# Optimization experiments

Measured on AMD Instinct MI355X. Metric: run time of the kernel, lower is better.

## Reference

```python
import jax, jax.numpy as jnp
import numpy as np

# Repo globals / config
VOCAB_SIZE = 14
TOK_DIM = 8
POS_DIM = 8
D_MODEL = TOK_DIM + POS_DIM  # 16
MAX_SEQ_LEN = 2048
N_HEADS = 2
HEAD_DIM = 3
ATTN_DIM = N_HEADS * HEAD_DIM  # 6
FFN_DIM = 3
B, T = 16, 2048
EPS = 1e-5


def _ln(x, w, b):
    m = jnp.mean(x, axis=-1, keepdims=True)
    v = jnp.var(x, axis=-1, keepdims=True)
    return (x - m) * jax.lax.rsqrt(v + EPS) * w + b


def setup_inputs() -> dict:
    key = jax.random.key(0)
    ks = jax.random.split(key, 20)
    g = lambda k, shape: (jax.random.normal(k, shape, jnp.float32) * 0.1)
    return {
        "idx": jax.random.randint(ks[0], (B, T), 0, VOCAB_SIZE),
        "tok_emb": g(ks[1], (VOCAB_SIZE, TOK_DIM)),
        "pos_enc": g(ks[2], (MAX_SEQ_LEN, POS_DIM)),
        "Wq": g(ks[3], (ATTN_DIM, POS_DIM)),
        "Wk": g(ks[4], (ATTN_DIM, POS_DIM)),
        "Wv": g(ks[5], (ATTN_DIM, TOK_DIM)),
        "Wo": g(ks[6], (D_MODEL, ATTN_DIM)),
        "ln1_w": jnp.ones((D_MODEL,), jnp.float32),
        "ln1_b": jnp.zeros((D_MODEL,), jnp.float32),
        "ln2_w": jnp.ones((D_MODEL,), jnp.float32),
        "ln2_b": jnp.zeros((D_MODEL,), jnp.float32),
        "lnf_w": jnp.ones((D_MODEL,), jnp.float32),
        "lnf_b": jnp.zeros((D_MODEL,), jnp.float32),
        "W1": g(ks[7], (FFN_DIM, D_MODEL)),
        "b1": jnp.zeros((FFN_DIM,), jnp.float32),
        "W2": g(ks[8], (D_MODEL, FFN_DIM)),
        "b2": jnp.zeros((D_MODEL,), jnp.float32),
        "Wh": g(ks[9], (TOK_DIM, D_MODEL)),
    }


def reference(idx, tok_emb, pos_enc, Wq, Wk, Wv, Wo,
              ln1_w, ln1_b, ln2_w, ln2_b, lnf_w, lnf_b,
              W1, b1, W2, b2, Wh):
    Bq, Tq = idx.shape
    tok = tok_emb[idx]                                  # [B,T,TOK_DIM]
    pos = jnp.broadcast_to(pos_enc[:Tq][None], (Bq, Tq, POS_DIM))
    x = jnp.concatenate([tok, pos], axis=-1)            # [B,T,D_MODEL]
    h = _ln(x, ln1_w, ln1_b)
    x_tok = h[..., :TOK_DIM]
    x_pos = h[..., TOK_DIM:]
    # projections (torch Linear: y = x @ W.T)
    q = (x_pos @ Wq.T).reshape(Bq, Tq, N_HEADS, HEAD_DIM).transpose(0, 2, 1, 3)
    k = (x_pos @ Wk.T).reshape(Bq, Tq, N_HEADS, HEAD_DIM).transpose(0, 2, 1, 3)
    v = (x_tok @ Wv.T).reshape(Bq, Tq, N_HEADS, HEAD_DIM).transpose(0, 2, 1, 3)
    scores = jnp.einsum('bhqd,bhkd->bhqk', q, k) / jnp.sqrt(jnp.float32(HEAD_DIM))
    mask = jnp.tril(jnp.ones((Tq, Tq), dtype=bool))
    scores = jnp.where(mask[None, None], scores, -jnp.inf)
    attn = jax.nn.softmax(scores, axis=-1)
    out = jnp.einsum('bhqk,bhkd->bhqd', attn, v)
    out = out.transpose(0, 2, 1, 3).reshape(Bq, Tq, ATTN_DIM)
    x = x + out @ Wo.T
    h2 = _ln(x, ln2_w, ln2_b)
    x = x + (jax.nn.gelu(h2 @ W1.T + b1, approximate=False) @ W2.T + b2)
    x = _ln(x, lnf_w, lnf_b)
    return (x @ Wh.T) @ tok_emb.T                       # tied head -> [B,T,VOCAB]
```

## Files before the change

### kernel.cpp

```cpp
#include <hip/hip_runtime.h>
#include <math.h>

#define BB    16
#define TT    2048
#define VOCAB 14
#define TOKD  8
#define POSD  8
#define DM    16
#define NH    2
#define HD    3
#define AD    6
#define FFND  3

#define NTOK  (BB*TT)
#define BH    (BB*NH)
#define TPB   36
#define NTILE (BH*TPB)

struct P {
    const int*   idx;
    const float* tok_emb;
    const float* pos_enc;
    const float* Wq;
    const float* Wk;
    const float* Wv;
    const float* Wo;
    const float* ln1w;
    const float* ln1b;
    const float* ln2w;
    const float* ln2b;
    const float* lnfw;
    const float* lnfb;
    const float* W1;
    const float* b1;
    const float* W2;
    const float* b2;
    const float* Wh;
    float*       out;
    float4*      pbuf;
};

__device__ __forceinline__ void ln1_of(const P& p, int b, int t, float* h) {
    float x[DM];
    int tok = p.idx[b * TT + t];
    #pragma unroll
    for (int j = 0; j < TOKD; ++j) x[j]        = p.tok_emb[tok * TOKD + j];
    #pragma unroll
    for (int j = 0; j < POSD; ++j) x[TOKD + j] = p.pos_enc[t * POSD + j];

    float m = 0.f;
    #pragma unroll
    for (int j = 0; j < DM; ++j) m += x[j];
    m *= (1.f / DM);
    float v = 0.f;
    #pragma unroll
    for (int j = 0; j < DM; ++j) { float d = x[j] - m; v += d * d; }
    v *= (1.f / DM);
    float rs = rsqrtf(v + 1e-5f);
    #pragma unroll
    for (int j = 0; j < DM; ++j)
        h[j] = (x[j] - m) * rs * p.ln1w[j] + p.ln1b[j];
}

#define LOADKV(it)                                                             \
    float4 Kr = skv[((kw + (it)) << 1)];                                       \
    float4 Vr = skv[((kw + (it)) << 1) + 1];                                   \
    float k0 = Kr.x, k1 = Kr.y, k2 = Kr.z;                                     \
    float v0 = Vr.x, v1 = Vr.y, v2 = Vr.z;

__global__ __launch_bounds__(256) void attn_kernel(P p) {
    __shared__ float4 skv[512];
    __shared__ float4 sq[256];
    __shared__ float4 spart[1024];

    const int tid  = threadIdx.x;
    int tile = blockIdx.x;
    int bh   = tile / TPB;
    int r    = tile - bh * TPB;
    int s    = 0;
    while (((s + 1) * (s + 2)) / 2 <= r) ++s;
    int c    = r - (s * (s + 1)) / 2;
    int b    = bh >> 1;
    int hh   = bh & 1;

    {
        float hK[DM];
        ln1_of(p, b, (c << 8) + tid, hK);
        float k0=0.f,k1=0.f,k2=0.f,v0=0.f,v1=0.f,v2=0.f;
        const float* wk = p.Wk + (hh * 3) * 8;
        const float* wv_ = p.Wv + (hh * 3) * 8;
        #pragma unroll
        for (int j = 0; j < 8; ++j) {
            k0 = fmaf(wk[j],      hK[TOKD + j], k0);
            k1 = fmaf(wk[8 + j],  hK[TOKD + j], k1);
            k2 = fmaf(wk[16 + j], hK[TOKD + j], k2);
            v0 = fmaf(wv_[j],      hK[j], v0);
            v1 = fmaf(wv_[8 + j],  hK[j], v1);
            v2 = fmaf(wv_[16 + j], hK[j], v2);
        }
        skv[(tid << 1)]     = make_float4(k0, k1, k2, 0.f);
        skv[(tid << 1) + 1] = make_float4(v0, v1, v2, 0.f);

        float hQ[DM];
        if (c != s) {
            ln1_of(p, b, (s << 8) + tid, hQ);
        } else {
            #pragma unroll
            for (int j = 0; j < DM; ++j) hQ[j] = hK[j];
        }
        const float QS = 1.4426950408889634f / 1.7320508075688772f;
        float q0=0.f,q1=0.f,q2=0.f;
        const float* wq = p.Wq + (hh * 3) * 8;
        #pragma unroll
        for (int j = 0; j < 8; ++j) {
            q0 = fmaf(wq[j],      hQ[TOKD + j], q0);
            q1 = fmaf(wq[8 + j],  hQ[TOKD + j], q1);
            q2 = fmaf(wq[16 + j], hQ[TOKD + j], q2);
        }
        sq[tid] = make_float4(q0 * QS, q1 * QS, q2 * QS, 0.f);
    }
    __syncthreads();

    int wv   = tid >> 6;
    int lane = tid & 63;
    int kw   = wv << 6;

    float4 qr[4];
    #pragma unroll
    for (int j = 0; j < 4; ++j) qr[j] = sq[(j << 6) + lane];

    float ac[4][4];
    #pragma unroll
    for (int j = 0; j < 4; ++j)
        ac[j][0] = ac[j][1] = ac[j][2] = ac[j][3] = 0.f;

    if (c < s) {
        #pragma unroll 4
        for (int it = 0; it < 64; ++it) {
            LOADKV(it)
            #pragma unroll
            for (int j = 0; j < 4; ++j) {
                float sc = fmaf(qr[j].x, k0, fmaf(qr[j].y, k1, qr[j].z * k2));
                float pr = __builtin_amdgcn_exp2f(sc);
                ac[j][0] = fmaf(pr, v0, ac[j][0]);
                ac[j][1] = fmaf(pr, v1, ac[j][1]);
                ac[j][2] = fmaf(pr, v2, ac[j][2]);
                ac[j][3] += pr;
            }
        }
    } else {
        #pragma unroll
        for (int j = 0; j < 4; ++j) {
            if (j < wv) continue;
            if (j == wv) {
                #pragma unroll 4
                for (int it = 0; it < 64; ++it) {
                    LOADKV(it)
                    float sc = fmaf(qr[j].x, k0, fmaf(qr[j].y, k1, qr[j].z * k2));
                    float pr = __builtin_amdgcn_exp2f(sc);
                    pr = (it <= lane) ? pr : 0.f;
                    ac[j][0] = fmaf(pr, v0, ac[j][0]);
                    ac[j][1] = fmaf(pr, v1, ac[j][1]);
                    ac[j][2] = fmaf(pr, v2, ac[j][2]);
                    ac[j][3] += pr;
                }
            } else {
                #pragma unroll 4
                for (int it = 0; it < 64; ++it) {
                    LOADKV(it)
                    float sc = fmaf(qr[j].x, k0, fmaf(qr[j].y, k1, qr[j].z * k2));
                    float pr = __builtin_amdgcn_exp2f(sc);
                    ac[j][0] = fmaf(pr, v0, ac[j][0]);
                    ac[j][1] = fmaf(pr, v1, ac[j][1]);
                    ac[j][2] = fmaf(pr, v2, ac[j][2]);
                    ac[j][3] += pr;
                }
            }
        }
    }

    #pragma unroll
    for (int j = 0; j < 4; ++j)
        spart[(wv << 8) + (j << 6) + lane] =
            make_float4(ac[j][0], ac[j][1], ac[j][2], ac[j][3]);
    __syncthreads();

    float4 p0 = spart[tid];
    float4 p1 = spart[256 + tid];
    float4 p2 = spart[512 + tid];
    float4 p3 = spart[768 + tid];
    float4 acc = make_float4(p0.x+p1.x+p2.x+p3.x, p0.y+p1.y+p2.y+p3.y,
                             p0.z+p1.z+p2.z+p3.z, p0.w+p1.w+p2.w+p3.w);
    p.pbuf[((size_t)bh * 8 + c) * TT + (s << 8) + tid] = acc;
}

__global__ __launch_bounds__(256) void epi_kernel(P p) {
    int gid = blockIdx.x * 256 + threadIdx.x;
    if (gid >= NTOK) return;
    int t = gid & (TT - 1);
    int b = gid >> 11;
    int s = t >> 8;

    float x[DM];
    int tok = p.idx[gid];
    #pragma unroll
    for (int j = 0; j < TOKD; ++j) x[j]        = p.tok_emb[tok * TOKD + j];
    #pragma unroll
    for (int j = 0; j < POSD; ++j) x[TOKD + j] = p.pos_enc[t * POSD + j];

    float att[AD];
    #pragma unroll
    for (int hh = 0; hh < NH; ++hh) {
        const float4* pp = p.pbuf + ((size_t)(b * NH + hh) * 8) * TT + t;
        float4 acc = pp[0];
        for (int c = 1; c <= s; ++c) {
            float4 e = pp[(size_t)c * TT];
            acc.x += e.x; acc.y += e.y; acc.z += e.z; acc.w += e.w;
        }
        float inv = 1.f / acc.w;
        att[hh*3+0] = acc.x * inv;
        att[hh*3+1] = acc.y * inv;
        att[hh*3+2] = acc.z * inv;
    }

    float xo[DM];
    #pragma unroll
    for (int j = 0; j < DM; ++j) {
        float sacc = x[j];
        #pragma unroll
        for (int a = 0; a < AD; ++a) sacc = fmaf(p.Wo[j * AD + a], att[a], sacc);
        xo[j] = sacc;
    }

    float m = 0.f;
    #pragma unroll
    for (int j = 0; j < DM; ++j) m += xo[j];
    m *= (1.f / DM);
    float v = 0.f;
    #pragma unroll
    for (int j = 0; j < DM; ++j) { float d = xo[j] - m; v += d * d; }
    v *= (1.f / DM);
    float rs = rsqrtf(v + 1e-5f);
    float h2[DM];
    #pragma unroll
    for (int j = 0; j < DM; ++j)
        h2[j] = (xo[j] - m) * rs * p.ln2w[j] + p.ln2b[j];

    float g[FFND];
    #pragma unroll
    for (int cc = 0; cc < FFND; ++cc) {
        float f = p.b1[cc];
        #pragma unroll
        for (int j = 0; j < DM; ++j) f = fmaf(p.W1[cc * DM + j], h2[j], f);
        g[cc] = 0.5f * f * (1.f + erff(f * 0.70710678118654752f));
    }
    float x2[DM];
    #pragma unroll
    for (int j = 0; j < DM; ++j) {
        float sacc = xo[j] + p.b2[j];
        #pragma unroll
        for (int cc = 0; cc < FFND; ++cc) sacc = fmaf(p.W2[j * FFND + cc], g[cc], sacc);
        x2[j] = sacc;
    }

    m = 0.f;
    #pragma unroll
    for (int j = 0; j < DM; ++j) m += x2[j];
    m *= (1.f / DM);
    v = 0.f;
    #pragma unroll
    for (int j = 0; j < DM; ++j) { float d = x2[j] - m; v += d * d; }
    v *= (1.f / DM);
    rs = rsqrtf(v + 1e-5f);
    float y[DM];
    #pragma unroll
    for (int j = 0; j < DM; ++j)
        y[j] = (x2[j] - m) * rs * p.lnfw[j] + p.lnfb[j];

    float t8[TOKD];
    #pragma unroll
    for (int pp = 0; pp < TOKD; ++pp) {
        float sacc = 0.f;
        #pragma unroll
        for (int j = 0; j < DM; ++j) sacc = fmaf(p.Wh[pp * DM + j], y[j], sacc);
        t8[pp] = sacc;
    }
    float* op = p.out + (size_t)gid * VOCAB;
    #pragma unroll
    for (int vcb = 0; vcb < VOCAB; ++vcb) {
        float sacc = 0.f;
        #pragma unroll
        for (int pp = 0; pp < TOKD; ++pp)
            sacc = fmaf(t8[pp], p.tok_emb[vcb * TOKD + pp], sacc);
        op[vcb] = sacc;
    }
}

extern "C" void kernel_launch(void* const* d_in, const int* in_sizes, int n_in,
                              void* d_out, int out_size, void* d_ws, size_t ws_size,
                              hipStream_t stream) {
    P p;
    p.idx     = (const int*)d_in[0];
    p.tok_emb = (const float*)d_in[1];
    p.pos_enc = (const float*)d_in[2];
    p.Wq      = (const float*)d_in[3];
    p.Wk      = (const float*)d_in[4];
    p.Wv      = (const float*)d_in[5];
    p.Wo      = (const float*)d_in[6];
    p.ln1w    = (const float*)d_in[7];
    p.ln1b    = (const float*)d_in[8];
    p.ln2w    = (const float*)d_in[9];
    p.ln2b    = (const float*)d_in[10];
    p.lnfw    = (const float*)d_in[11];
    p.lnfb    = (const float*)d_in[12];
    p.W1      = (const float*)d_in[13];
    p.b1      = (const float*)d_in[14];
    p.W2      = (const float*)d_in[15];
    p.b2      = (const float*)d_in[16];
    p.Wh      = (const float*)d_in[17];
    p.out     = (float*)d_out;
    p.pbuf    = (float4*)d_ws;

    attn_kernel<<<NTILE, 256, 0, stream>>>(p);
    epi_kernel<<<NTOK / 256, 256, 0, stream>>>(p);
}
```

Before: 127.1 us.

## Broadcast K/V via readlane from registers instead of shared memory

Keys and values computed per thread stay in registers, and each wave broadcasts them to its lanes with readlane instead of staging them through LDS. This removes the LDS writes and per-iteration LDS loads of K/V. The diagonal tile loop now runs all four query groups with a mask instead of skipping the blocks below the diagonal, so it does more exp work there. Readlane needs a uniform lane index, which fully unrolled loops should provide; partial unrolling may force a scalar or loop-indexed path.

```diff
diff --git a/kernel.cpp b/kernel.cpp
--- a/kernel.cpp
+++ b/kernel.cpp
@@ -62,14 +62,11 @@
         h[j] = (x[j] - m) * rs * p.ln1w[j] + p.ln1b[j];
 }
 
-#define LOADKV(it)                                                             \
-    float4 Kr = skv[((kw + (it)) << 1)];                                       \
-    float4 Vr = skv[((kw + (it)) << 1) + 1];                                   \
-    float k0 = Kr.x, k1 = Kr.y, k2 = Kr.z;                                     \
-    float v0 = Vr.x, v1 = Vr.y, v2 = Vr.z;
+__device__ __forceinline__ float RL(float x, int it) {
+    return __uint_as_float(__builtin_amdgcn_readlane(__float_as_uint(x), it));
+}
 
 __global__ __launch_bounds__(256) void attn_kernel(P p) {
-    __shared__ float4 skv[512];
     __shared__ float4 sq[256];
     __shared__ float4 spart[1024];
 
@@ -83,11 +80,15 @@
     int b    = bh >> 1;
     int hh   = bh & 1;
 
+    int wv   = tid >> 6;
+    int lane = tid & 63;
+
+    float rk0, rk1, rk2, rv0, rv1, rv2;
     {
         float hK[DM];
         ln1_of(p, b, (c << 8) + tid, hK);
         float k0=0.f,k1=0.f,k2=0.f,v0=0.f,v1=0.f,v2=0.f;
-        const float* wk = p.Wk + (hh * 3) * 8;
+        const float* wk  = p.Wk + (hh * 3) * 8;
         const float* wv_ = p.Wv + (hh * 3) * 8;
         #pragma unroll
         for (int j = 0; j < 8; ++j) {
@@ -98,8 +99,7 @@
             v1 = fmaf(wv_[8 + j],  hK[j], v1);
             v2 = fmaf(wv_[16 + j], hK[j], v2);
         }
-        skv[(tid << 1)]     = make_float4(k0, k1, k2, 0.f);
-        skv[(tid << 1) + 1] = make_float4(v0, v1, v2, 0.f);
+        rk0 = k0; rk1 = k1; rk2 = k2; rv0 = v0; rv1 = v1; rv2 = v2;
 
         float hQ[DM];
         if (c != s) {
@@ -121,10 +121,6 @@
     }
     __syncthreads();
 
-    int wv   = tid >> 6;
-    int lane = tid & 63;
-    int kw   = wv << 6;
-
     float4 qr[4];
     #pragma unroll
     for (int j = 0; j < 4; ++j) qr[j] = sq[(j << 6) + lane];
@@ -137,7 +133,8 @@
     if (c < s) {
         #pragma unroll 4
         for (int it = 0; it < 64; ++it) {
-            LOADKV(it)
+            float k0 = RL(rk0, it), k1 = RL(rk1, it), k2 = RL(rk2, it);
+            float v0 = RL(rv0, it), v1 = RL(rv1, it), v2 = RL(rv2, it);
             #pragma unroll
             for (int j = 0; j < 4; ++j) {
                 float sc = fmaf(qr[j].x, k0, fmaf(qr[j].y, k1, qr[j].z * k2));
@@ -149,32 +146,21 @@
             }
         }
     } else {
-        #pragma unroll
-        for (int j = 0; j < 4; ++j) {
-            if (j < wv) continue;
-            if (j == wv) {
-                #pragma unroll 4
-                for (int it = 0; it < 64; ++it) {
-                    LOADKV(it)
-                    float sc = fmaf(qr[j].x, k0, fmaf(qr[j].y, k1, qr[j].z * k2));
-                    float pr = __builtin_amdgcn_exp2f(sc);
-                    pr = (it <= lane) ? pr : 0.f;
-                    ac[j][0] = fmaf(pr, v0, ac[j][0]);
-                    ac[j][1] = fmaf(pr, v1, ac[j][1]);
-                    ac[j][2] = fmaf(pr, v2, ac[j][2]);
-                    ac[j][3] += pr;
-                }
-            } else {
-                #pragma unroll 4
-                for (int it = 0; it < 64; ++it) {
-                    LOADKV(it)
-                    float sc = fmaf(qr[j].x, k0, fmaf(qr[j].y, k1, qr[j].z * k2));
-                    float pr = __builtin_amdgcn_exp2f(sc);
-                    ac[j][0] = fmaf(pr, v0, ac[j][0]);
-                    ac[j][1] = fmaf(pr, v1, ac[j][1]);
-                    ac[j][2] = fmaf(pr, v2, ac[j][2]);
-                    ac[j][3] += pr;
-                }
+        int kwv = wv << 6;
+        #pragma unroll 4
+        for (int it = 0; it < 64; ++it) {
+            float k0 = RL(rk0, it), k1 = RL(rk1, it), k2 = RL(rk2, it);
+            float v0 = RL(rv0, it), v1 = RL(rv1, it), v2 = RL(rv2, it);
+            int keyloc = kwv + it;
+            #pragma unroll
+            for (int j = 0; j < 4; ++j) {
+                float sc = fmaf(qr[j].x, k0, fmaf(qr[j].y, k1, qr[j].z * k2));
+                float pr = __builtin_amdgcn_exp2f(sc);
+                pr = (keyloc <= ((j << 6) + lane)) ? pr : 0.f;
+                ac[j][0] = fmaf(pr, v0, ac[j][0]);
+                ac[j][1] = fmaf(pr, v1, ac[j][1]);
+                ac[j][2] = fmaf(pr, v2, ac[j][2]);
+                ac[j][3] += pr;
             }
         }
     }
```

New measurement: 131.0 us. 1.03x slower.
